# Optimization experiments

Hardware: AMD Instinct MI355X
Metric: run time of the kernel (lower is better)

The kernel has to match this reference:

```python
import jax, jax.numpy as jnp
import numpy as np

H = 8          # num_heads
NUM_SEEDS = 4  # num_seeds (T = T0 + NUM_SEEDS in training/non_trivial)
NEG_INF = float('-inf')


def setup_inputs() -> dict:
    key = jax.random.key(0)
    ks = jax.random.split(key, 9)
    B, T, L, C = 4, 16, 64, 512
    T0 = T - NUM_SEEDS
    x = jax.random.normal(ks[0], (B, T0 * L, C), dtype=jnp.float32)
    x_ctx = jax.random.normal(ks[1], (B, T, L, C), dtype=jnp.float32)
    dx_ctx = jax.random.normal(ks[2], (B, T, L, C), dtype=jnp.float32)
    ctx_mask = jax.random.randint(ks[3], (B, T), 0, 2).astype(jnp.bool_)
    s = 1.0 / np.sqrt(C)
    qkv_w = jax.random.normal(ks[4], (3 * C, C), dtype=jnp.float32) * s
    k_w = jax.random.normal(ks[5], (C, C), dtype=jnp.float32) * s
    v_w = jax.random.normal(ks[6], (C, C), dtype=jnp.float32) * s
    proj_w = jax.random.normal(ks[7], (C, C), dtype=jnp.float32) * s
    proj_b = jax.random.normal(ks[8], (C,), dtype=jnp.float32) * 0.01
    return {"x": x, "x_ctx": x_ctx, "dx_ctx": dx_ctx, "ctx_mask": ctx_mask,
            "qkv_w": qkv_w, "k_w": k_w, "v_w": v_w, "proj_w": proj_w,
            "proj_b": proj_b}


def reference(x, x_ctx, dx_ctx, ctx_mask, qkv_w, k_w, v_w, proj_w, proj_b):
    B, T, L, C = x_ctx.shape
    T0 = x.shape[1] // L
    hd = C // H
    scale = hd ** (-0.5)

    # qkv for the current (self) tokens: [3, B, H, T0*L, hd]
    qkv = (x @ qkv_w.T).reshape(B, T0 * L, 3, H, hd).transpose(2, 0, 3, 1, 4)
    q, k, v = qkv[0], qkv[1], qkv[2]

    # context keys/values: [B, H, T*L, hd]
    k_ctx = (dx_ctx.reshape(B, T * L, C) @ k_w.T).reshape(B, T * L, H, hd).transpose(0, 2, 1, 3)
    v_ctx = (x_ctx.reshape(B, T * L, C) @ v_w.T).reshape(B, T * L, H, hd).transpose(0, 2, 1, 3)

    # cross-context scores: [B, H, T0*L, T, L]
    attn = (jnp.einsum('bhqd,bhkd->bhqk', q, k_ctx) * scale).reshape(B, H, T0 * L, T, L)

    # context mask: drop whole context frames where ctx_mask is False
    attn = jnp.where(ctx_mask[:, None, None, :, None], attn, NEG_INF)

    # non-trivial temporal mask (training): query frame i can't attend to
    # context frame i + num_seeds
    nt = (jnp.arange(T0)[:, None] + NUM_SEEDS) == jnp.arange(T)[None, :]  # [T0, T]
    attn6 = attn.reshape(B, H, T0, L, T, L)
    attn6 = jnp.where(nt[None, None, :, None, :, None], NEG_INF, attn6)
    attn = attn6.reshape(B, H, T0 * L, T, L)

    # per-frame self attention scores: [B, H, T0, L, L] -> [B, H, T0*L, 1, L]
    q6 = q.reshape(B, H, T0, L, hd)
    k6 = k.reshape(B, H, T0, L, hd)
    self_attn = (jnp.einsum('bhtqd,bhtkd->bhtqk', q6, k6) * scale).reshape(B, H, T0 * L, 1, L)

    # joint softmax over (T+1)*L keys
    attn = jnp.concatenate([attn, self_attn], axis=-2).reshape(B, H, T0 * L, (T + 1) * L)
    attn = jax.nn.softmax(attn, axis=-1)

    # split back: cross part @ v_ctx, self part @ v (per frame)
    out = jnp.einsum('bhqk,bhkd->bhqd', attn[:, :, :, :-L], v_ctx)
    a_self = attn[:, :, :, -L:].reshape(B, H, T0, L, L)
    v6 = v.reshape(B, H, T0, L, hd)
    out = out + jnp.einsum('bhtqk,bhtkd->bhtqd', a_self, v6).reshape(B, H, T0 * L, hd)

    out = out.transpose(0, 2, 1, 3).reshape(B, T0 * L, C)
    return out @ proj_w.T + proj_b
```

## Files before the change

### kernel.cpp

```cpp
#include <hip/hip_runtime.h>
#include <hip/hip_bf16.h>

typedef __attribute__((ext_vector_type(8))) short bf16x8;
typedef __attribute__((ext_vector_type(4))) float f32x4;

#define BB 4
#define TT 16
#define NT0 12
#define LL 64
#define CC 512
#define HH 8
#define HD 64
#define NQ (NT0*LL)
#define NCTX (TT*LL)

#define GPTR(x) ((__attribute__((address_space(1))) void*)(x))
#define SPTR(x) ((__attribute__((address_space(3))) void*)(x))
#define VMCNT(n) (((n) & 15) | (((n) >> 4) << 14) | (7u << 4) | (0xFu << 8))

__device__ __forceinline__ float bf2f(ushort u) {
  union { unsigned int i; float f; } x; x.i = ((unsigned int)u) << 16; return x.f;
}
__device__ __forceinline__ ushort f2bf(float f) {
  union { float f; unsigned int i; } x; x.f = f;
  unsigned int r = x.i + 0x7fffu + ((x.i >> 16) & 1u);
  return (ushort)(r >> 16);
}

__global__ __launch_bounds__(256) void cvt_all(const float* __restrict__ w0,
                                               const float* __restrict__ w1,
                                               const float* __restrict__ w2,
                                               const float* __restrict__ w3,
                                               const float* __restrict__ x,
                                               const float* __restrict__ xc,
                                               const float* __restrict__ dxc,
                                               ushort* __restrict__ dst) {
  long i = (long)blockIdx.x * 256 + threadIdx.x;
  const float* src; long off;
  if (i < 196608)       { src = w0;  off = 0; }
  else if (i < 262144)  { src = w1;  off = 196608; }
  else if (i < 327680)  { src = w2;  off = 262144; }
  else if (i < 393216)  { src = w3;  off = 327680; }
  else if (i < 786432)  { src = x;   off = 393216; }
  else if (i < 1310720) { src = xc;  off = 786432; }
  else                  { src = dxc; off = 1310720; }
  f32x4 v = *(const f32x4*)(src + (i - off) * 4);
  ushort4 o = { f2bf(v[0]), f2bf(v[1]), f2bf(v[2]), f2bf(v[3]) };
  *(ushort4*)(dst + i * 4) = o;
}

__device__ __forceinline__ void gemm128_mac(const ushort* __restrict__ A,
                                            const ushort* __restrict__ W,
                                            int mt, int nt, ushort* lds,
                                            f32x4* acc) {
  int t = threadIdx.x;
  int p0 = t, p1 = t + 256;
  int r0 = p0 >> 2, r1 = p1 >> 2;
  int c0 = (p0 & 3) ^ ((r0 >> 1) & 3);
  int c1 = (p1 & 3) ^ ((r1 >> 1) & 3);
  const ushort* ga0 = A + (size_t)(mt * 128 + r0) * 512 + c0 * 8;
  const ushort* ga1 = A + (size_t)(mt * 128 + r1) * 512 + c1 * 8;
  const ushort* gw0 = W + (size_t)(nt * 128 + r0) * 512 + c0 * 8;
  const ushort* gw1 = W + (size_t)(nt * 128 + r1) * 512 + c1 * 8;

  int lane = t & 63, l15 = lane & 15, kg = lane >> 4;
  int wv = t >> 6;
  int mh = (wv >> 1) * 64, nh = (wv & 1) * 64;
  int swz = kg ^ ((l15 >> 1) & 3);
  int faoff = (mh + l15) * 32 + swz * 8;
  int fwoff = (nh + l15) * 32 + swz * 8;

  __builtin_amdgcn_global_load_lds(GPTR(ga0), SPTR(lds + p0 * 8), 16, 0, 0);
  __builtin_amdgcn_global_load_lds(GPTR(ga1), SPTR(lds + p1 * 8), 16, 0, 0);
  __builtin_amdgcn_global_load_lds(GPTR(gw0), SPTR(lds + 4096 + p0 * 8), 16, 0, 0);
  __builtin_amdgcn_global_load_lds(GPTR(gw1), SPTR(lds + 4096 + p1 * 8), 16, 0, 0);

#pragma unroll
  for (int ks = 0; ks < 16; ++ks) {
    int cur = (ks & 1) * 8192;
    int nxt = 8192 - cur;
    if (ks < 15) {
      int ko = (ks + 1) * 32;
      __builtin_amdgcn_global_load_lds(GPTR(ga0 + ko), SPTR(lds + nxt + p0 * 8), 16, 0, 0);
      __builtin_amdgcn_global_load_lds(GPTR(ga1 + ko), SPTR(lds + nxt + p1 * 8), 16, 0, 0);
      __builtin_amdgcn_global_load_lds(GPTR(gw0 + ko), SPTR(lds + nxt + 4096 + p0 * 8), 16, 0, 0);
      __builtin_amdgcn_global_load_lds(GPTR(gw1 + ko), SPTR(lds + nxt + 4096 + p1 * 8), 16, 0, 0);
      __builtin_amdgcn_s_waitcnt(VMCNT(4));
    } else {
      __builtin_amdgcn_s_waitcnt(VMCNT(0));
    }
    asm volatile("" ::: "memory");
    __builtin_amdgcn_s_barrier();
    asm volatile("" ::: "memory");

    const ushort* fa = lds + cur + faoff;
    const ushort* fw = lds + cur + 4096 + fwoff;
    bf16x8 af[4], wf[4];
#pragma unroll
    for (int i = 0; i < 4; ++i) af[i] = *(const bf16x8*)(fa + i * 512);
#pragma unroll
    for (int i = 0; i < 4; ++i) wf[i] = *(const bf16x8*)(fw + i * 512);
#pragma unroll
    for (int mi = 0; mi < 4; ++mi)
#pragma unroll
      for (int ni = 0; ni < 4; ++ni)
        acc[mi * 4 + ni] =
            __builtin_amdgcn_mfma_f32_16x16x32_bf16(af[mi], wf[ni], acc[mi * 4 + ni], 0, 0, 0);

    asm volatile("" ::: "memory");
    __builtin_amdgcn_s_barrier();
    asm volatile("" ::: "memory");
  }
}

template<int OUTMODE>
__device__ __forceinline__ void gemm128(const ushort* __restrict__ A,
                                        const ushort* __restrict__ W,
                                        ushort* __restrict__ C,
                                        ushort* __restrict__ CT,
                                        float* __restrict__ Cf,
                                        const float* __restrict__ bias,
                                        int mt, int nt, int N, long TM,
                                        ushort* lds) {
  f32x4 acc[16] = {{0,0,0,0},{0,0,0,0},{0,0,0,0},{0,0,0,0},
                   {0,0,0,0},{0,0,0,0},{0,0,0,0},{0,0,0,0},
                   {0,0,0,0},{0,0,0,0},{0,0,0,0},{0,0,0,0},
                   {0,0,0,0},{0,0,0,0},{0,0,0,0},{0,0,0,0}};
  gemm128_mac(A, W, mt, nt, lds, acc);

  int lane = threadIdx.x & 63, l15 = lane & 15, kg = lane >> 4;
  int wv = threadIdx.x >> 6;
  int Rw = mt * 128 + (wv >> 1) * 64;
  int Cw = nt * 128 + (wv & 1) * 64;
#pragma unroll
  for (int mi = 0; mi < 4; ++mi) {
    int row = Rw + mi * 16 + kg * 4;
#pragma unroll
    for (int ni = 0; ni < 4; ++ni) {
      f32x4 v = acc[mi * 4 + ni];
      int col = Cw + ni * 16 + l15;
      if (OUTMODE == 0) {
#pragma unroll
        for (int r = 0; r < 4; ++r) C[(size_t)(row + r) * N + col] = f2bf(v[r]);
      } else if (OUTMODE == 1) {
        ushort4 o = { f2bf(v[0]), f2bf(v[1]), f2bf(v[2]), f2bf(v[3]) };
        *(ushort4*)(CT + (long)col * TM + row) = o;
      } else {
        float bv = bias[col];
#pragma unroll
        for (int r = 0; r < 4; ++r) Cf[(size_t)(row + r) * N + col] = v[r] + bv;
      }
    }
  }
}

__global__ __launch_bounds__(256) void gemm3(const ushort* __restrict__ xb,
                                             const ushort* __restrict__ dxb,
                                             const ushort* __restrict__ xcb,
                                             const ushort* __restrict__ qkvwb,
                                             const ushort* __restrict__ kwb,
                                             const ushort* __restrict__ vwb,
                                             ushort* __restrict__ qkv,
                                             ushort* __restrict__ vselfT,
                                             ushort* __restrict__ kctx,
                                             ushort* __restrict__ vctxT) {
  __shared__ ushort lds[16384];
  int blk = blockIdx.x;
  if (blk < 288) {
    int mt = blk % 24, nt = blk / 24;
    if (nt < 8)
      gemm128<0>(xb, qkvwb, qkv, nullptr, nullptr, nullptr, mt, nt, 1536, 0, lds);
    else
      gemm128<1>(xb, qkvwb, nullptr, vselfT - (size_t)1024 * 3072, nullptr, nullptr,
                 mt, nt, 1536, 3072, lds);
  } else if (blk < 416) {
    int r = blk - 288;
    gemm128<0>(dxb, kwb, kctx, nullptr, nullptr, nullptr, r % 32, r / 32, 512, 0, lds);
  } else {
    int r = blk - 416;
    gemm128<1>(xcb, vwb, nullptr, vctxT, nullptr, nullptr, r % 32, r / 32, 512, 4096, lds);
  }
}

__global__ __launch_bounds__(256) void gemm_proj(const ushort* __restrict__ aout,
                                                 const ushort* __restrict__ pwb,
                                                 const float* __restrict__ bias,
                                                 float* __restrict__ out) {
  __shared__ ushort lds[16384];
  int blk = blockIdx.x;
  gemm128<2>(aout, pwb, nullptr, nullptr, out, bias, blk % 24, blk / 24, 512, 0, lds);
}

__device__ __forceinline__ void attn_tile(const ushort* __restrict__ kbase, int kstr,
                                          const ushort* __restrict__ vtb, int vtN,
                                          bf16x8 q0, bf16x8 q1,
                                          int l15, int kg,
                                          ushort* __restrict__ myPt,
                                          f32x4* acc, float& Lacc) {
  f32x4 s[4];
#pragma unroll
  for (int st = 0; st < 4; ++st) {
    const ushort* kp = kbase + (size_t)(st * 16 + l15) * kstr + kg * 8;
    bf16x8 k0 = *(const bf16x8*)kp;
    bf16x8 k1 = *(const bf16x8*)(kp + 32);
    f32x4 z = {0, 0, 0, 0};
    z = __builtin_amdgcn_mfma_f32_16x16x32_bf16(k0, q0, z, 0, 0, 0);
    z = __builtin_amdgcn_mfma_f32_16x16x32_bf16(k1, q1, z, 0, 0, 0);
    s[st] = z;
  }
#pragma unroll
  for (int st = 0; st < 4; ++st) {
    float p0 = __builtin_exp2f(fmaf(s[st][0], 0.18033688f, -23.0831206f));
    float p1 = __builtin_exp2f(fmaf(s[st][1], 0.18033688f, -23.0831206f));
    float p2 = __builtin_exp2f(fmaf(s[st][2], 0.18033688f, -23.0831206f));
    float p3 = __builtin_exp2f(fmaf(s[st][3], 0.18033688f, -23.0831206f));
    Lacc += (p0 + p1) + (p2 + p3);
    ushort4 pk = { f2bf(p0), f2bf(p1), f2bf(p2), f2bf(p3) };
    *(ushort4*)(myPt + l15 * 72 + st * 16 + kg * 4) = pk;
  }
#pragma unroll
  for (int kc = 0; kc < 2; ++kc) {
    bf16x8 pb = *(const bf16x8*)(myPt + l15 * 72 + kc * 32 + kg * 8);
#pragma unroll
    for (int d = 0; d < 4; ++d) {
      const ushort* vp = vtb + (size_t)(d * 16 + l15) * vtN + kc * 32 + kg * 8;
      bf16x8 vf = *(const bf16x8*)vp;
      acc[d] = __builtin_amdgcn_mfma_f32_16x16x32_bf16(vf, pb, acc[d], 0, 0, 0);
    }
  }
}

__global__ __launch_bounds__(512) void flash_attn(const ushort* __restrict__ qkv,
                                                  const ushort* __restrict__ kctx,
                                                  const ushort* __restrict__ vctxT,
                                                  const ushort* __restrict__ vselfT,
                                                  const int* __restrict__ ctx_mask,
                                                  ushort* __restrict__ aout) {
  __shared__ ushort sm[18432];
  int blk = blockIdx.x;
  int qh = blk & 1;
  int rest = blk >> 1;
  int t0 = rest % NT0;
  int h  = (rest / NT0) % HH;
  int b  = rest / (NT0 * HH);
  int tid = threadIdx.x, wv = tid >> 6, lane = tid & 63;
  int qg = wv & 1, ks = wv >> 1;
  int l15 = lane & 15, kg = lane >> 4;

  int qrow = b * NQ + t0 * LL + qh * 32 + qg * 16 + l15;
  const ushort* qp = qkv + (size_t)qrow * 1536 + h * HD + kg * 8;
  bf16x8 q0 = *(const bf16x8*)qp;
  bf16x8 q1 = *(const bf16x8*)(qp + 32);

  f32x4 acc[4] = {{0,0,0,0},{0,0,0,0},{0,0,0,0},{0,0,0,0}};
  float Lacc = 0.f;
  ushort* Pt0 = sm + wv * 2304;

  int kts[4]; int nkt = 0;
#pragma unroll
  for (int ki = 0; ki < 4; ++ki) {
    int kt = ks * 4 + ki;
    if (ctx_mask[b * TT + kt] != 0 && kt != t0 + 4) kts[nkt++] = kt;
  }

  const ushort* vctxb = vctxT + (size_t)h * HD * (BB * NCTX) + b * NCTX;
  int buf = 0;
  for (int ki = 0; ki < nkt; ++ki) {
    int kt = kts[ki];
    attn_tile(kctx + (size_t)(b * NCTX + kt * LL) * CC + h * HD, CC,
              vctxb + kt * LL, BB * NCTX,
              q0, q1, l15, kg, Pt0 + buf * 1152, acc, Lacc);
    buf ^= 1;
  }
  if (ks == 0) {
    attn_tile(qkv + (size_t)(b * NQ + t0 * LL) * 1536 + CC + h * HD, 1536,
              vselfT + (size_t)h * HD * (BB * NQ) + b * NQ + t0 * LL, BB * NQ,
              q0, q1, l15, kg, Pt0 + buf * 1152, acc, Lacc);
  }

  float Lr = Lacc;
  Lr += __shfl_xor(Lr, 16, 64);
  Lr += __shfl_xor(Lr, 32, 64);

  __syncthreads();
  float* fsm = (float*)sm;
  if (ks) {
    float* reg = fsm + (size_t)(qg * 3 + ks - 1) * 1088;
#pragma unroll
    for (int d = 0; d < 4; ++d) *(f32x4*)(reg + lane * 16 + d * 4) = acc[d];
    reg[1024 + lane] = Lr;
  }
  __syncthreads();
  if (!ks) {
    float Ls = Lr;
    f32x4 o[4];
#pragma unroll
    for (int d = 0; d < 4; ++d) o[d] = acc[d];
#pragma unroll
    for (int j = 0; j < 3; ++j) {
      const float* reg = fsm + (size_t)(qg * 3 + j) * 1088;
      Ls += reg[1024 + lane];
#pragma unroll
      for (int d = 0; d < 4; ++d)
        o[d] += *(const f32x4*)(reg + lane * 16 + d * 4);
    }
    float inv = 1.f / Ls;
    int orow = b * NQ + t0 * LL + qh * 32 + qg * 16 + l15;
#pragma unroll
    for (int d = 0; d < 4; ++d) {
      ushort4 ov = { f2bf(o[d][0] * inv), f2bf(o[d][1] * inv),
                     f2bf(o[d][2] * inv), f2bf(o[d][3] * inv) };
      *(ushort4*)(aout + (size_t)orow * CC + h * HD + d * 16 + kg * 4) = ov;
    }
  }
}

extern "C" void kernel_launch(void* const* d_in, const int* in_sizes, int n_in,
                              void* d_out, int out_size, void* d_ws, size_t ws_size,
                              hipStream_t stream) {
  const float* x        = (const float*)d_in[0];
  const float* x_ctx    = (const float*)d_in[1];
  const float* dx_ctx   = (const float*)d_in[2];
  const int*   ctx_mask = (const int*)d_in[3];
  const float* qkv_w    = (const float*)d_in[4];
  const float* k_w      = (const float*)d_in[5];
  const float* v_w      = (const float*)d_in[6];
  const float* proj_w   = (const float*)d_in[7];
  const float* proj_b   = (const float*)d_in[8];
  float* out = (float*)d_out;

  ushort* ws = (ushort*)d_ws;
  ushort* qkvwb  = ws;
  ushort* kwb    = ws + 786432;
  ushort* vwb    = ws + 1048576;
  ushort* pwb    = ws + 1310720;
  ushort* xb     = ws + 1572864;
  ushort* xcb    = ws + 3145728;
  ushort* dxb    = ws + 5242880;
  ushort* qkv    = ws + 7340032;
  ushort* kctx   = ws + 12058624;
  ushort* vctxT  = ws + 14155776;
  ushort* vselfT = ws + 16252928;
  ushort* aout   = ws + 17825792;

  cvt_all<<<7168, 256, 0, stream>>>(qkv_w, k_w, v_w, proj_w, x, x_ctx, dx_ctx, ws);
  gemm3<<<544, 256, 0, stream>>>(xb, dxb, xcb, qkvwb, kwb, vwb,
                                 qkv, vselfT, kctx, vctxT);
  flash_attn<<<768, 512, 0, stream>>>(qkv, kctx, vctxT, vselfT, ctx_mask, aout);
  gemm_proj<<<96, 256, 0, stream>>>(aout, pwb, proj_b, out);
}
```

Baseline: 145.7 us.

## Triple-buffer GEMM K-loop and use 64-row tiles for output projection

Turns the bf16 GEMM mainloop into a templated version with three LDS stages: loads run two k-steps ahead, and the vmcnt waits are adjusted to match. The output projection GEMM switches to 64x128 tiles, so 192 blocks launch instead of 96 and more CUs get work. The goal is to hide global load latency and to fill the device better for the small projection GEMM. In exchange, LDS use per block rises, which may lower occupancy for gemm3. The VMCNT macro also drops its high-bit encoding.

Measured after the change: 144.1 us. About the same (-1.1%).

```diff
diff --git a/kernel.cpp b/kernel.cpp
--- a/kernel.cpp
+++ b/kernel.cpp
@@ -16,7 +16,7 @@
 
 #define GPTR(x) ((__attribute__((address_space(1))) void*)(x))
 #define SPTR(x) ((__attribute__((address_space(3))) void*)(x))
-#define VMCNT(n) (((n) & 15) | (((n) >> 4) << 14) | (7u << 4) | (0xFu << 8))
+#define VMCNT(n) (((n) & 15) | (7u << 4) | (0xFu << 8))
 
 __device__ __forceinline__ float bf2f(ushort u) {
   union { unsigned int i; float f; } x; x.i = ((unsigned int)u) << 16; return x.f;
@@ -49,43 +49,54 @@
   *(ushort4*)(dst + i * 4) = o;
 }
 
-__device__ __forceinline__ void gemm128_mac(const ushort* __restrict__ A,
-                                            const ushort* __restrict__ W,
-                                            int mt, int nt, ushort* lds,
-                                            f32x4* acc) {
+template<int MT>
+__device__ __forceinline__ void gemm_mac(const ushort* __restrict__ A,
+                                         const ushort* __restrict__ W,
+                                         int mt, int nt, ushort* lds,
+                                         f32x4* acc) {
+  constexpr int ACH = MT * 4;
+  constexpr int ASZ = MT * 32;
+  constexpr int BUF = ASZ + 4096;
+  constexpr int L   = (MT == 128) ? 4 : 3;
+
   int t = threadIdx.x;
-  int p0 = t, p1 = t + 256;
-  int r0 = p0 >> 2, r1 = p1 >> 2;
-  int c0 = (p0 & 3) ^ ((r0 >> 1) & 3);
-  int c1 = (p1 & 3) ^ ((r1 >> 1) & 3);
-  const ushort* ga0 = A + (size_t)(mt * 128 + r0) * 512 + c0 * 8;
-  const ushort* ga1 = A + (size_t)(mt * 128 + r1) * 512 + c1 * 8;
-  const ushort* gw0 = W + (size_t)(nt * 128 + r0) * 512 + c0 * 8;
-  const ushort* gw1 = W + (size_t)(nt * 128 + r1) * 512 + c1 * 8;
+  int pa0 = t, pa1 = t + 256;
+  int ra0 = pa0 >> 2, ra1 = pa1 >> 2;
+  int ca0 = (pa0 & 3) ^ ((ra0 >> 1) & 3);
+  int ca1 = (pa1 & 3) ^ ((ra1 >> 1) & 3);
+  int pw0 = t, pw1 = t + 256;
+  const ushort* ga0 = A + (size_t)(mt * MT + ra0) * 512 + ca0 * 8;
+  const ushort* ga1 = A + (size_t)(mt * MT + ra1) * 512 + ca1 * 8;
+  const ushort* gw0 = W + (size_t)(nt * 128 + ra0) * 512 + ca0 * 8;
+  const ushort* gw1 = W + (size_t)(nt * 128 + ra1) * 512 + ca1 * 8;
 
   int lane = t & 63, l15 = lane & 15, kg = lane >> 4;
   int wv = t >> 6;
-  int mh = (wv >> 1) * 64, nh = (wv & 1) * 64;
+  int mh = (wv >> 1) * (MT / 2), nh = (wv & 1) * 64;
   int swz = kg ^ ((l15 >> 1) & 3);
   int faoff = (mh + l15) * 32 + swz * 8;
   int fwoff = (nh + l15) * 32 + swz * 8;
 
-  __builtin_amdgcn_global_load_lds(GPTR(ga0), SPTR(lds + p0 * 8), 16, 0, 0);
-  __builtin_amdgcn_global_load_lds(GPTR(ga1), SPTR(lds + p1 * 8), 16, 0, 0);
-  __builtin_amdgcn_global_load_lds(GPTR(gw0), SPTR(lds + 4096 + p0 * 8), 16, 0, 0);
-  __builtin_amdgcn_global_load_lds(GPTR(gw1), SPTR(lds + 4096 + p1 * 8), 16, 0, 0);
+  auto stage = [&](int ks, int bb) {
+    int ko = ks * 32;
+    __builtin_amdgcn_global_load_lds(GPTR(ga0 + ko), SPTR(lds + bb + pa0 * 8), 16, 0, 0);
+    if (MT == 128)
+      __builtin_amdgcn_global_load_lds(GPTR(ga1 + ko), SPTR(lds + bb + pa1 * 8), 16, 0, 0);
+    __builtin_amdgcn_global_load_lds(GPTR(gw0 + ko), SPTR(lds + bb + ASZ + pw0 * 8), 16, 0, 0);
+    __builtin_amdgcn_global_load_lds(GPTR(gw1 + ko), SPTR(lds + bb + ASZ + pw1 * 8), 16, 0, 0);
+  };
+
+  stage(0, 0);
+  stage(1, BUF);
 
 #pragma unroll
   for (int ks = 0; ks < 16; ++ks) {
-    int cur = (ks & 1) * 8192;
-    int nxt = 8192 - cur;
-    if (ks < 15) {
-      int ko = (ks + 1) * 32;
-      __builtin_amdgcn_global_load_lds(GPTR(ga0 + ko), SPTR(lds + nxt + p0 * 8), 16, 0, 0);
-      __builtin_amdgcn_global_load_lds(GPTR(ga1 + ko), SPTR(lds + nxt + p1 * 8), 16, 0, 0);
-      __builtin_amdgcn_global_load_lds(GPTR(gw0 + ko), SPTR(lds + nxt + 4096 + p0 * 8), 16, 0, 0);
-      __builtin_amdgcn_global_load_lds(GPTR(gw1 + ko), SPTR(lds + nxt + 4096 + p1 * 8), 16, 0, 0);
-      __builtin_amdgcn_s_waitcnt(VMCNT(4));
+    int cur = (ks % 3) * BUF;
+    if (ks < 14) {
+      stage(ks + 2, ((ks + 2) % 3) * BUF);
+      __builtin_amdgcn_s_waitcnt(VMCNT(2 * L));
+    } else if (ks == 14) {
+      __builtin_amdgcn_s_waitcnt(VMCNT(L));
     } else {
       __builtin_amdgcn_s_waitcnt(VMCNT(0));
     }
@@ -94,14 +105,14 @@
     asm volatile("" ::: "memory");
 
     const ushort* fa = lds + cur + faoff;
-    const ushort* fw = lds + cur + 4096 + fwoff;
-    bf16x8 af[4], wf[4];
-#pragma unroll
-    for (int i = 0; i < 4; ++i) af[i] = *(const bf16x8*)(fa + i * 512);
+    const ushort* fw = lds + cur + ASZ + fwoff;
+    bf16x8 af[MT / 32], wf[4];
+#pragma unroll
+    for (int i = 0; i < MT / 32; ++i) af[i] = *(const bf16x8*)(fa + i * 512);
 #pragma unroll
     for (int i = 0; i < 4; ++i) wf[i] = *(const bf16x8*)(fw + i * 512);
 #pragma unroll
-    for (int mi = 0; mi < 4; ++mi)
+    for (int mi = 0; mi < MT / 32; ++mi)
 #pragma unroll
       for (int ni = 0; ni < 4; ++ni)
         acc[mi * 4 + ni] =
@@ -113,27 +124,26 @@
   }
 }
 
-template<int OUTMODE>
-__device__ __forceinline__ void gemm128(const ushort* __restrict__ A,
-                                        const ushort* __restrict__ W,
-                                        ushort* __restrict__ C,
-                                        ushort* __restrict__ CT,
-                                        float* __restrict__ Cf,
-                                        const float* __restrict__ bias,
-                                        int mt, int nt, int N, long TM,
-                                        ushort* lds) {
-  f32x4 acc[16] = {{0,0,0,0},{0,0,0,0},{0,0,0,0},{0,0,0,0},
-                   {0,0,0,0},{0,0,0,0},{0,0,0,0},{0,0,0,0},
-                   {0,0,0,0},{0,0,0,0},{0,0,0,0},{0,0,0,0},
-                   {0,0,0,0},{0,0,0,0},{0,0,0,0},{0,0,0,0}};
-  gemm128_mac(A, W, mt, nt, lds, acc);
+template<int MT, int OUTMODE>
+__device__ __forceinline__ void gemm_body(const ushort* __restrict__ A,
+                                          const ushort* __restrict__ W,
+                                          ushort* __restrict__ C,
+                                          ushort* __restrict__ CT,
+                                          float* __restrict__ Cf,
+                                          const float* __restrict__ bias,
+                                          int mt, int nt, int N, long TM,
+                                          ushort* lds) {
+  f32x4 acc[(MT / 32) * 4];
+#pragma unroll
+  for (int i = 0; i < (MT / 32) * 4; ++i) acc[i] = (f32x4){0, 0, 0, 0};
+  gemm_mac<MT>(A, W, mt, nt, lds, acc);
 
   int lane = threadIdx.x & 63, l15 = lane & 15, kg = lane >> 4;
   int wv = threadIdx.x >> 6;
-  int Rw = mt * 128 + (wv >> 1) * 64;
+  int Rw = mt * MT + (wv >> 1) * (MT / 2);
   int Cw = nt * 128 + (wv & 1) * 64;
 #pragma unroll
-  for (int mi = 0; mi < 4; ++mi) {
+  for (int mi = 0; mi < MT / 32; ++mi) {
     int row = Rw + mi * 16 + kg * 4;
 #pragma unroll
     for (int ni = 0; ni < 4; ++ni) {
@@ -164,21 +174,21 @@
                                              ushort* __restrict__ vselfT,
                                              ushort* __restrict__ kctx,
                                              ushort* __restrict__ vctxT) {
-  __shared__ ushort lds[16384];
+  __shared__ ushort lds[24576];
   int blk = blockIdx.x;
   if (blk < 288) {
     int mt = blk % 24, nt = blk / 24;
     if (nt < 8)
-      gemm128<0>(xb, qkvwb, qkv, nullptr, nullptr, nullptr, mt, nt, 1536, 0, lds);
+      gemm_body<128, 0>(xb, qkvwb, qkv, nullptr, nullptr, nullptr, mt, nt, 1536, 0, lds);
     else
-      gemm128<1>(xb, qkvwb, nullptr, vselfT - (size_t)1024 * 3072, nullptr, nullptr,
-                 mt, nt, 1536, 3072, lds);
+      gemm_body<128, 1>(xb, qkvwb, nullptr, vselfT - (size_t)1024 * 3072, nullptr, nullptr,
+                        mt, nt, 1536, 3072, lds);
   } else if (blk < 416) {
     int r = blk - 288;
-    gemm128<0>(dxb, kwb, kctx, nullptr, nullptr, nullptr, r % 32, r / 32, 512, 0, lds);
+    gemm_body<128, 0>(dxb, kwb, kctx, nullptr, nullptr, nullptr, r % 32, r / 32, 512, 0, lds);
   } else {
     int r = blk - 416;
-    gemm128<1>(xcb, vwb, nullptr, vctxT, nullptr, nullptr, r % 32, r / 32, 512, 4096, lds);
+    gemm_body<128, 1>(xcb, vwb, nullptr, vctxT, nullptr, nullptr, r % 32, r / 32, 512, 4096, lds);
   }
 }
 
@@ -186,9 +196,9 @@
                                                  const ushort* __restrict__ pwb,
                                                  const float* __restrict__ bias,
                                                  float* __restrict__ out) {
-  __shared__ ushort lds[16384];
+  __shared__ ushort lds[18432];
   int blk = blockIdx.x;
-  gemm128<2>(aout, pwb, nullptr, nullptr, out, bias, blk % 24, blk / 24, 512, 0, lds);
+  gemm_body<64, 2>(aout, pwb, nullptr, nullptr, out, bias, blk % 48, blk / 48, 512, 0, lds);
 }
 
 __device__ __forceinline__ void attn_tile(const ushort* __restrict__ kbase, int kstr,
@@ -347,5 +357,5 @@
   gemm3<<<544, 256, 0, stream>>>(xb, dxb, xcb, qkvwb, kwb, vwb,
                                  qkv, vselfT, kctx, vctxT);
   flash_attn<<<768, 512, 0, stream>>>(qkv, kctx, vctxT, vselfT, ctx_mask, aout);
-  gemm_proj<<<96, 256, 0, stream>>>(aout, pwb, proj_b, out);
-}
+  gemm_proj<<<192, 256, 0, stream>>>(aout, pwb, proj_b, out);
+}
```
